# Optimization experiments

Hardware: AMD Instinct MI355X
Metric: run time of the kernel (lower is better)

Reference implementation:

```python
import jax, jax.numpy as jnp
import numpy as np

C, H, W_DIM, B, N = 9, 260, 346, 16, 32768
E = B * N
HIDDEN = 100
NEG_SLOPE = 0.1


def setup_inputs() -> dict:
    key = jax.random.key(0)
    ks = jax.random.split(key, 10)
    xs = jax.random.randint(ks[0], (E,), 0, W_DIM, dtype=jnp.int32)
    ys = jax.random.randint(ks[1], (E,), 0, H, dtype=jnp.int32)
    ts = jax.random.uniform(ks[2], (E,), dtype=jnp.float32)
    ps = jax.random.randint(ks[3], (E,), 0, 2, dtype=jnp.int32)  # polarity already mapped to {0,1}
    bs = jnp.repeat(jnp.arange(B, dtype=jnp.int32), N)           # batch id per event
    W1 = jax.random.normal(ks[4], (HIDDEN, 1), dtype=jnp.float32) * 0.5
    b1 = jax.random.normal(ks[5], (HIDDEN,), dtype=jnp.float32) * 0.1
    W2 = jax.random.normal(ks[6], (HIDDEN, HIDDEN), dtype=jnp.float32) * 0.1
    b2 = jax.random.normal(ks[7], (HIDDEN,), dtype=jnp.float32) * 0.1
    W3 = jax.random.normal(ks[8], (1, HIDDEN), dtype=jnp.float32) * 0.1
    b3 = jax.random.normal(ks[9], (1,), dtype=jnp.float32) * 0.1
    return {"xs": xs, "ys": ys, "ts": ts, "ps": ps, "bs": bs,
            "W1": W1, "b1": b1, "W2": W2, "b2": b2, "W3": W3, "b3": b3}


def _lrelu(v):
    return jnp.where(v >= 0, v, NEG_SLOPE * v)


def _value_layer(t, W1, b1, W2, b2, W3, b3):
    # ValueLayer MLP: scalar per event -> hidden -> hidden -> scalar
    h = _lrelu(t[:, None] * W1[:, 0][None, :] + b1)  # [E, HIDDEN]
    h = _lrelu(h @ W2.T + b2)                        # [E, HIDDEN]
    return (h @ W3.T + b3)[:, 0]                     # [E]


def reference(xs, ys, ts, ps, bs, W1, b1, W2, b2, W3, b3):
    num_voxels = 2 * C * H * W_DIM * B
    # idx = x + W*y + W*H*C*p + W*H*C*2*b  (+ W*H*i_bin per bin)
    idx0 = xs + W_DIM * ys + (W_DIM * H * C) * ps + (2 * W_DIM * H * C) * bs
    vox = jnp.zeros((num_voxels,), dtype=ts.dtype)
    for i_bin in range(C):  # fixed small loop over temporal bins
        vals = ts * _value_layer(ts - i_bin / (C - 1), W1, b1, W2, b2, W3, b3)
        idx = jnp.clip(idx0 + (W_DIM * H) * i_bin, 0, num_voxels - 1)
        vox = vox.at[idx].add(vals)
    vox = vox.reshape(B, 2, C, H, W_DIM)
    # concat polarity channels -> [B, 2C, H, W]
    return jnp.concatenate([vox[:, 0], vox[:, 1]], axis=1)
```

## Files before the change

kernel.cpp:

```cpp
#include <hip/hip_runtime.h>

#define C_BINS 9
#define H_DIM 260
#define WDIM 346
#define B_DIM 16
#define N_PER_B 32768
#define HIDDEN 100
#define NEG_SLOPE 0.1f
#define WH (WDIM * H_DIM)
#define NUM_VOXELS (2 * C_BINS * WH * B_DIM)
#define TABLE_N 16384
#define HALF_N (TABLE_N / 2)
#define BIN_SHIFT (TABLE_N / 16)
#define T9_STRIDE 12

#define ROWS_PER_TILE 4
#define TILES_PER_BP 65
#define LBUCKETS (2 * TILES_PER_BP)
#define NBUCKETS (B_DIM * LBUCKETS)
#define BUCKET_CAP 512
#define EV_PER_BLOCK 1024
#define TILE_ELEMS (C_BINS * ROWS_PER_TILE * WDIM)
#define TILE_F4 (TILE_ELEMS / 4)
#define CHUNK_F4 (ROWS_PER_TILE * WDIM / 4)
#define BUILD_BLOCKS (TABLE_N / 32 + 1)

#define SMEM_BYTES 41632
#define SM_STAGE 0
#define SM_SCAN  8192
#define SM_LCNT  10240
#define SM_LPRE  10760
#define SM_GBASE 11280
#define SM_SLB   11800

#define WS_TABLE_OFF 0
#define WS_COUNT_OFF 66048
#define WS_T9_OFF    74752
#define WS_REC_OFF   468480
#define WS_REC_SZ    ((size_t)NBUCKETS * BUCKET_CAP * 8)
#define WS_NEEDED    (WS_REC_OFF + WS_REC_SZ)

__global__ __launch_bounds__(256) void fused_build_bucket_kernel(
    const int* __restrict__ xs, const int* __restrict__ ys,
    const float* __restrict__ ts, const int* __restrict__ ps,
    const float* __restrict__ W1, const float* __restrict__ b1,
    const float* __restrict__ W2, const float* __restrict__ b2,
    const float* __restrict__ W3, const float* __restrict__ b3,
    float* __restrict__ table, float* __restrict__ t9,
    unsigned int* __restrict__ counts,
    unsigned long long* __restrict__ records,
    int E, int n_bucket_blocks, int write_t9)
{
    __shared__ __align__(16) char smem[SMEM_BYTES];
    const int tid = threadIdx.x;

    if (blockIdx.x < (unsigned)n_bucket_blocks) {
        unsigned long long* stage = (unsigned long long*)(smem + SM_STAGE);
        unsigned*      scan  = (unsigned*)(smem + SM_SCAN);
        unsigned*      lcnt  = (unsigned*)(smem + SM_LCNT);
        unsigned*      lpre  = (unsigned*)(smem + SM_LPRE);
        unsigned*      gbase = (unsigned*)(smem + SM_GBASE);
        unsigned char* slb   = (unsigned char*)(smem + SM_SLB);

        const int e0 = blockIdx.x * EV_PER_BLOCK;
        const int b  = e0 >> 15;

        for (int i = tid; i < LBUCKETS; i += 256) lcnt[i] = 0;
        __syncthreads();

        int lb[4];
        unsigned rank[4];
        unsigned long long rec[4];
        const int eb = e0 + tid * 4;
        if (eb + 3 < E) {
            const int v4 = (e0 >> 2) + tid;
            const int4   xv = ((const int4*)xs)[v4];
            const int4   yv = ((const int4*)ys)[v4];
            const int4   pv = ((const int4*)ps)[v4];
            const float4 tv = ((const float4*)ts)[v4];
            const int   xa[4] = {xv.x, xv.y, xv.z, xv.w};
            const int   ya[4] = {yv.x, yv.y, yv.z, yv.w};
            const int   pa[4] = {pv.x, pv.y, pv.z, pv.w};
            const float ta[4] = {tv.x, tv.y, tv.z, tv.w};
#pragma unroll
            for (int j = 0; j < 4; ++j) {
                const int yt = ya[j] >> 2;
                const int yl = ya[j] & 3;
                lb[j]  = pa[j] * TILES_PER_BP + yt;
                rec[j] = ((unsigned long long)__float_as_uint(ta[j]) << 32)
                       | (unsigned)(yl * WDIM + xa[j]);
                rank[j] = atomicAdd(&lcnt[lb[j]], 1u);
            }
        } else {
#pragma unroll
            for (int j = 0; j < 4; ++j) {
                const int e = eb + j;
                if (e < E) {
                    const int   x = xs[e];
                    const int   y = ys[e];
                    const int   p = ps[e];
                    const float t = ts[e];
                    const int  yt = y >> 2;
                    const int  yl = y & 3;
                    lb[j]  = p * TILES_PER_BP + yt;
                    rec[j] = ((unsigned long long)__float_as_uint(t) << 32)
                           | (unsigned)(yl * WDIM + x);
                    rank[j] = atomicAdd(&lcnt[lb[j]], 1u);
                } else {
                    lb[j] = -1;
                }
            }
        }
        __syncthreads();

        scan[tid] = (tid < LBUCKETS) ? lcnt[tid] : 0u;
        __syncthreads();
        int src = 0;
        for (int off = 1; off < 256; off <<= 1) {
            unsigned v = scan[src * 256 + tid];
            if (tid >= off) v += scan[src * 256 + tid - off];
            scan[(src ^ 1) * 256 + tid] = v;
            src ^= 1;
            __syncthreads();
        }
        if (tid < LBUCKETS) {
            const unsigned c = lcnt[tid];
            lpre[tid]  = scan[src * 256 + tid] - c;
            gbase[tid] = c ? atomicAdd(&counts[b * LBUCKETS + tid], c) : 0u;
        }
        __syncthreads();

#pragma unroll
        for (int j = 0; j < 4; ++j) {
            if (lb[j] >= 0) {
                const unsigned s = lpre[lb[j]] + rank[j];
                stage[s] = rec[j];
                slb[s]   = (unsigned char)lb[j];
            }
        }
        __syncthreads();

        const int nblk = (E - e0 < EV_PER_BLOCK) ? (E - e0) : EV_PER_BLOCK;
        for (int s = tid; s < nblk; s += 256) {
            const int l = slb[s];
            const unsigned ofs = gbase[l] + ((unsigned)s - lpre[l]);
            if (ofs < BUCKET_CAP)
                records[(size_t)(b * LBUCKETS + l) * BUCKET_CAP + ofs] = stage[s];
        }
    } else {
        float* sW2 = (float*)smem;
        float* sW1 = (float*)(smem + 40032);
        float* sb1 = sW1 + HIDDEN;
        float* sb2 = sb1 + HIDDEN;
        float* sW3 = sb2 + HIDDEN;

        {
            const float4* __restrict__ srcw = (const float4*)W2;
            float4* dst = (float4*)sW2;
            for (int i = tid; i < (HIDDEN * HIDDEN) / 4; i += 256) dst[i] = srcw[i];
        }
        if (tid < 8) sW2[HIDDEN * HIDDEN + tid] = 0.0f;
        if (tid < HIDDEN) {
            sW1[tid] = W1[tid];
            sb1[tid] = b1[tid];
            sb2[tid] = b2[tid];
            sW3[tid] = W3[tid];
        }
        __syncthreads();

        const int entry_local = tid >> 3;
        const int o  = tid & 7;
        const int q  = o & 3;
        const int j0 = (o >> 2) * 52;
        const int g  = (blockIdx.x - n_bucket_blocks) * 32 + entry_local;
        if (g > TABLE_N) return;
        const float u = -1.0f + (2.0f / (float)TABLE_N) * (float)g;

        float h1[52];
#pragma unroll
        for (int j = 0; j < 52; ++j) {
            const int jj = j0 + j;
            float v = (jj < HIDDEN) ? fmaf(u, sW1[jj], sb1[jj]) : 0.0f;
            h1[j] = (v >= 0.0f) ? v : NEG_SLOPE * v;
        }

        float acc = 0.0f;
        for (int k = q; k < HIDDEN; k += 4) {
            const float* __restrict__ row = &sW2[k * HIDDEN + j0];
            float a0 = 0.f, a1 = 0.f, a2 = 0.f, a3 = 0.f;
#pragma unroll
            for (int j = 0; j < 52; j += 4) {
                a0 = fmaf(row[j + 0], h1[j + 0], a0);
                a1 = fmaf(row[j + 1], h1[j + 1], a1);
                a2 = fmaf(row[j + 2], h1[j + 2], a2);
                a3 = fmaf(row[j + 3], h1[j + 3], a3);
            }
            float part = (a0 + a1) + (a2 + a3);
            part += __shfl_xor(part, 4);
            float a = sb2[k] + part;
            a = (a >= 0.0f) ? a : NEG_SLOPE * a;
            acc = fmaf(a, sW3[k], acc);
        }
        acc += __shfl_xor(acc, 1);
        acc += __shfl_xor(acc, 2);
        if (o == 0) {
            const float val = acc + b3[0];
            table[g] = val;
            if (write_t9) {
#pragma unroll
                for (int i = 0; i < C_BINS; ++i) {
                    const int r = g - HALF_N + BIN_SHIFT * i;
                    if (r >= 0 && r <= HALF_N) t9[r * T9_STRIDE + i] = val;
                }
            }
        }
    }
}

__global__ __launch_bounds__(512) void tile_kernel(
    const unsigned int* __restrict__ counts, const uint2* __restrict__ records,
    const float* __restrict__ t9, float* __restrict__ out)
{
    __shared__ __align__(16) float tile[TILE_ELEMS];
    const int tid = threadIdx.x;
    const int bucket = blockIdx.x;
    const int yt = bucket % TILES_PER_BP;
    const int bp = bucket / TILES_PER_BP;

    const int n = min(counts[bucket], (unsigned)BUCKET_CAP);
    const uint2* __restrict__ rec = records + (size_t)bucket * BUCKET_CAP;

    float4* __restrict__ t4 = (float4*)tile;
    {
        const float4 z = {0.f, 0.f, 0.f, 0.f};
        for (int k = tid; k < TILE_F4; k += 512) t4[k] = z;
    }
    __syncthreads();

    for (int r = tid; r < n; r += 512) {
        const uint2 v = rec[r];
        const int   pix = (int)v.x;
        const float t   = __uint_as_float(v.y);
        const float pos = (t + 1.0f) * ((float)TABLE_N * 0.5f);
        const int   i0  = (int)pos;
        const float frac = pos - (float)i0;
        const int   rr  = i0 - HALF_N;
        const float4* __restrict__ rowp = (const float4*)(t9 + rr * T9_STRIDE);
        const float4 a0 = rowp[0], a1 = rowp[1], a2 = rowp[2];
        const float4 c0 = rowp[3], c1 = rowp[4], c2 = rowp[5];
        const float t0v[9] = {a0.x, a0.y, a0.z, a0.w, a1.x, a1.y, a1.z, a1.w, a2.x};
        const float t1v[9] = {c0.x, c0.y, c0.z, c0.w, c1.x, c1.y, c1.z, c1.w, c2.x};
#pragma unroll
        for (int i = 0; i < C_BINS; ++i) {
            const float val = t * fmaf(frac, t1v[i] - t0v[i], t0v[i]);
            atomicAdd(&tile[i * (ROWS_PER_TILE * WDIM) + pix], val);
        }
    }
    __syncthreads();

    float* __restrict__ obase = out + (size_t)bp * (C_BINS * WH)
                              + yt * (ROWS_PER_TILE * WDIM);
    for (int s = tid; s < TILE_F4; s += 512) {
        const int i = s / CHUNK_F4;
        const int k = s - i * CHUNK_F4;
        ((float4*)(obase + i * WH))[k] = t4[i * CHUNK_F4 + k];
    }
}

__global__ __launch_bounds__(256) void zero_kernel(float4* __restrict__ out, int n4)
{
    int i = blockIdx.x * 256 + threadIdx.x;
    int stride = gridDim.x * 256;
    float4 z = {0.f, 0.f, 0.f, 0.f};
    for (; i < n4; i += stride) out[i] = z;
}

__global__ __launch_bounds__(256) void scatter_kernel(
    const int* __restrict__ xs, const int* __restrict__ ys,
    const float* __restrict__ ts, const int* __restrict__ ps,
    const int* __restrict__ bs, const float* __restrict__ table,
    float* __restrict__ out, int E)
{
    const int e = blockIdx.x * 256 + threadIdx.x;
    if (e >= E) return;
    const int x = xs[e], y = ys[e], p = ps[e], b = bs[e];
    const float t = ts[e];
    int idx0 = x + WDIM * y + (WH * C_BINS) * p + (2 * WH * C_BINS) * b;
#pragma unroll
    for (int i = 0; i < C_BINS; ++i) {
        float u   = t - (float)i * (1.0f / (float)(C_BINS - 1));
        float pos = (u + 1.0f) * ((float)TABLE_N * 0.5f);
        int   i0  = (int)pos;
        i0 = (i0 < 0) ? 0 : ((i0 > TABLE_N - 1) ? TABLE_N - 1 : i0);
        float frac = pos - (float)i0;
        float f  = fmaf(frac, table[i0 + 1] - table[i0], table[i0]);
        int idx = idx0 + WH * i;
        idx = (idx < 0) ? 0 : ((idx >= NUM_VOXELS) ? NUM_VOXELS - 1 : idx);
        atomicAdd(&out[idx], t * f);
    }
}

extern "C" void kernel_launch(void* const* d_in, const int* in_sizes, int n_in,
                              void* d_out, int out_size, void* d_ws, size_t ws_size,
                              hipStream_t stream)
{
    const int*   xs = (const int*)d_in[0];
    const int*   ys = (const int*)d_in[1];
    const float* ts = (const float*)d_in[2];
    const int*   ps = (const int*)d_in[3];
    const int*   bs = (const int*)d_in[4];
    const float* W1 = (const float*)d_in[5];
    const float* b1 = (const float*)d_in[6];
    const float* W2 = (const float*)d_in[7];
    const float* b2 = (const float*)d_in[8];
    const float* W3 = (const float*)d_in[9];
    const float* b3 = (const float*)d_in[10];

    float* out = (float*)d_out;
    char*  ws  = (char*)d_ws;
    float* table = (float*)(ws + WS_TABLE_OFF);
    unsigned int* counts = (unsigned int*)(ws + WS_COUNT_OFF);
    float* t9 = (float*)(ws + WS_T9_OFF);
    const int E = in_sizes[0];
    const int use_fast = (ws_size >= WS_NEEDED) ? 1 : 0;

    if (use_fast) {
        unsigned long long* records = (unsigned long long*)(ws + WS_REC_OFF);
        const int nbB = (E + EV_PER_BLOCK - 1) / EV_PER_BLOCK;
        hipMemsetAsync(counts, 0, NBUCKETS * sizeof(unsigned int), stream);
        fused_build_bucket_kernel<<<nbB + BUILD_BLOCKS, 256, 0, stream>>>(
            xs, ys, ts, ps, W1, b1, W2, b2, W3, b3,
            table, t9, counts, records, E, nbB, 1);
        tile_kernel<<<NBUCKETS, 512, 0, stream>>>(
            counts, (const uint2*)records, t9, out);
    } else {
        fused_build_bucket_kernel<<<BUILD_BLOCKS, 256, 0, stream>>>(
            xs, ys, ts, ps, W1, b1, W2, b2, W3, b3,
            table, t9, counts, (unsigned long long*)out , E, 0, 0);
        zero_kernel<<<1024, 256, 0, stream>>>((float4*)out, out_size / 4);
        scatter_kernel<<<(E + 255) / 256, 256, 0, stream>>>(
            xs, ys, ts, ps, bs, table, out, E);
    }
}
```

Baseline: 172.7 us.

## Replace global bucket counters with per-block sorted segments and prefix offsets

The bucketing pass no longer reserves space in fixed-capacity global buckets with atomics. Each block now writes its locally sorted 1024 records contiguously, using coalesced 16-byte stores, plus a small per-block prefix table of bucket offsets. The tile kernel assigns 16 lanes to each of the 32 source blocks of its batch and reads that block's segment for the bucket. This removes the memset, the global atomics and the bucket-cap overflow truncation. In exchange, reads in the tile kernel are more fragmented, only 16 lanes work per segment, and the fast path is now restricted to the exact event count.

```diff
diff --git a/kernel.cpp b/kernel.cpp
--- a/kernel.cpp
+++ b/kernel.cpp
@@ -18,8 +18,9 @@
 #define TILES_PER_BP 65
 #define LBUCKETS (2 * TILES_PER_BP)
 #define NBUCKETS (B_DIM * LBUCKETS)
-#define BUCKET_CAP 512
 #define EV_PER_BLOCK 1024
+#define BLOCKS_PER_BATCH (N_PER_B / EV_PER_BLOCK)
+#define PRE_STRIDE 132
 #define TILE_ELEMS (C_BINS * ROWS_PER_TILE * WDIM)
 #define TILE_F4 (TILE_ELEMS / 4)
 #define CHUNK_F4 (ROWS_PER_TILE * WDIM / 4)
@@ -30,14 +31,12 @@
 #define SM_SCAN  8192
 #define SM_LCNT  10240
 #define SM_LPRE  10760
-#define SM_GBASE 11280
-#define SM_SLB   11800
 
 #define WS_TABLE_OFF 0
-#define WS_COUNT_OFF 66048
-#define WS_T9_OFF    74752
-#define WS_REC_OFF   468480
-#define WS_REC_SZ    ((size_t)NBUCKETS * BUCKET_CAP * 8)
+#define WS_T9_OFF    66048
+#define WS_PRE_OFF   459392
+#define WS_REC_OFF   614400
+#define WS_REC_SZ    ((size_t)B_DIM * N_PER_B * 8)
 #define WS_NEEDED    (WS_REC_OFF + WS_REC_SZ)
 
 __global__ __launch_bounds__(256) void fused_build_bucket_kernel(
@@ -47,23 +46,21 @@
     const float* __restrict__ W2, const float* __restrict__ b2,
     const float* __restrict__ W3, const float* __restrict__ b3,
     float* __restrict__ table, float* __restrict__ t9,
-    unsigned int* __restrict__ counts,
+    unsigned short* __restrict__ pre,
     unsigned long long* __restrict__ records,
-    int E, int n_bucket_blocks, int write_t9)
+    int E, int n_bucket_blocks)
 {
     __shared__ __align__(16) char smem[SMEM_BYTES];
     const int tid = threadIdx.x;
 
     if (blockIdx.x < (unsigned)n_bucket_blocks) {
         unsigned long long* stage = (unsigned long long*)(smem + SM_STAGE);
-        unsigned*      scan  = (unsigned*)(smem + SM_SCAN);
-        unsigned*      lcnt  = (unsigned*)(smem + SM_LCNT);
-        unsigned*      lpre  = (unsigned*)(smem + SM_LPRE);
-        unsigned*      gbase = (unsigned*)(smem + SM_GBASE);
-        unsigned char* slb   = (unsigned char*)(smem + SM_SLB);
-
-        const int e0 = blockIdx.x * EV_PER_BLOCK;
-        const int b  = e0 >> 15;
+        unsigned* scan = (unsigned*)(smem + SM_SCAN);
+        unsigned* lcnt = (unsigned*)(smem + SM_LCNT);
+        unsigned* lpre = (unsigned*)(smem + SM_LPRE);
+
+        const int g  = blockIdx.x;
+        const int e0 = g * EV_PER_BLOCK;
 
         for (int i = tid; i < LBUCKETS; i += 256) lcnt[i] = 0;
         __syncthreads();
@@ -123,29 +120,29 @@
             src ^= 1;
             __syncthreads();
         }
-        if (tid < LBUCKETS) {
-            const unsigned c = lcnt[tid];
-            lpre[tid]  = scan[src * 256 + tid] - c;
-            gbase[tid] = c ? atomicAdd(&counts[b * LBUCKETS + tid], c) : 0u;
-        }
+        const int nblk = (E - e0 < EV_PER_BLOCK) ? (E - e0) : EV_PER_BLOCK;
+        if (tid < LBUCKETS)
+            lpre[tid] = scan[src * 256 + tid] - lcnt[tid];
+        if (tid <= LBUCKETS)
+            pre[g * PRE_STRIDE + tid] =
+                (unsigned short)((tid < LBUCKETS) ? (scan[src * 256 + tid] - lcnt[tid])
+                                                  : (unsigned)nblk);
         __syncthreads();
 
 #pragma unroll
         for (int j = 0; j < 4; ++j) {
-            if (lb[j] >= 0) {
-                const unsigned s = lpre[lb[j]] + rank[j];
-                stage[s] = rec[j];
-                slb[s]   = (unsigned char)lb[j];
-            }
-        }
-        __syncthreads();
-
-        const int nblk = (E - e0 < EV_PER_BLOCK) ? (E - e0) : EV_PER_BLOCK;
-        for (int s = tid; s < nblk; s += 256) {
-            const int l = slb[s];
-            const unsigned ofs = gbase[l] + ((unsigned)s - lpre[l]);
-            if (ofs < BUCKET_CAP)
-                records[(size_t)(b * LBUCKETS + l) * BUCKET_CAP + ofs] = stage[s];
+            if (lb[j] >= 0) stage[lpre[lb[j]] + rank[j]] = rec[j];
+        }
+        __syncthreads();
+
+        unsigned long long* __restrict__ dst = records + (size_t)g * EV_PER_BLOCK;
+        if (nblk == EV_PER_BLOCK) {
+            ulonglong2* __restrict__ d2 = (ulonglong2*)dst;
+            const ulonglong2* __restrict__ s2 = (const ulonglong2*)stage;
+#pragma unroll
+            for (int s = tid; s < EV_PER_BLOCK / 2; s += 256) d2[s] = s2[s];
+        } else {
+            for (int s = tid; s < nblk; s += 256) dst[s] = stage[s];
         }
     } else {
         float* sW2 = (float*)smem;
@@ -206,29 +203,34 @@
         if (o == 0) {
             const float val = acc + b3[0];
             table[g] = val;
-            if (write_t9) {
-#pragma unroll
-                for (int i = 0; i < C_BINS; ++i) {
-                    const int r = g - HALF_N + BIN_SHIFT * i;
-                    if (r >= 0 && r <= HALF_N) t9[r * T9_STRIDE + i] = val;
-                }
+#pragma unroll
+            for (int i = 0; i < C_BINS; ++i) {
+                const int r = g - HALF_N + BIN_SHIFT * i;
+                if (r >= 0 && r <= HALF_N) t9[r * T9_STRIDE + i] = val;
             }
         }
     }
 }
 
 __global__ __launch_bounds__(512) void tile_kernel(
-    const unsigned int* __restrict__ counts, const uint2* __restrict__ records,
+    const unsigned short* __restrict__ pre, const uint2* __restrict__ records,
     const float* __restrict__ t9, float* __restrict__ out)
 {
     __shared__ __align__(16) float tile[TILE_ELEMS];
     const int tid = threadIdx.x;
     const int bucket = blockIdx.x;
-    const int yt = bucket % TILES_PER_BP;
-    const int bp = bucket / TILES_PER_BP;
-
-    const int n = min(counts[bucket], (unsigned)BUCKET_CAP);
-    const uint2* __restrict__ rec = records + (size_t)bucket * BUCKET_CAP;
+    const int b = bucket / LBUCKETS;
+    const int l = bucket - b * LBUCKETS;
+    const int p  = (l >= TILES_PER_BP) ? 1 : 0;
+    const int yt = l - p * TILES_PER_BP;
+    const int bp = b * 2 + p;
+
+    const int seg  = tid >> 4;
+    const int lane = tid & 15;
+    const int g    = b * BLOCKS_PER_BATCH + seg;
+    const int lo   = pre[g * PRE_STRIDE + l];
+    const int hi   = pre[g * PRE_STRIDE + l + 1];
+    const uint2* __restrict__ segrec = records + (size_t)g * EV_PER_BLOCK;
 
     float4* __restrict__ t4 = (float4*)tile;
     {
@@ -237,8 +239,8 @@
     }
     __syncthreads();
 
-    for (int r = tid; r < n; r += 512) {
-        const uint2 v = rec[r];
+    for (int r = lo + lane; r < hi; r += 16) {
+        const uint2 v = segrec[r];
         const int   pix = (int)v.x;
         const float t   = __uint_as_float(v.y);
         const float pos = (t + 1.0f) * ((float)TABLE_N * 0.5f);
@@ -319,24 +321,23 @@
     float* out = (float*)d_out;
     char*  ws  = (char*)d_ws;
     float* table = (float*)(ws + WS_TABLE_OFF);
-    unsigned int* counts = (unsigned int*)(ws + WS_COUNT_OFF);
     float* t9 = (float*)(ws + WS_T9_OFF);
+    unsigned short* pre = (unsigned short*)(ws + WS_PRE_OFF);
     const int E = in_sizes[0];
-    const int use_fast = (ws_size >= WS_NEEDED) ? 1 : 0;
+    const int use_fast = (ws_size >= WS_NEEDED) && (E == B_DIM * N_PER_B);
 
     if (use_fast) {
         unsigned long long* records = (unsigned long long*)(ws + WS_REC_OFF);
-        const int nbB = (E + EV_PER_BLOCK - 1) / EV_PER_BLOCK;
-        hipMemsetAsync(counts, 0, NBUCKETS * sizeof(unsigned int), stream);
+        const int nbB = E / EV_PER_BLOCK;
         fused_build_bucket_kernel<<<nbB + BUILD_BLOCKS, 256, 0, stream>>>(
             xs, ys, ts, ps, W1, b1, W2, b2, W3, b3,
-            table, t9, counts, records, E, nbB, 1);
+            table, t9, pre, records, E, nbB);
         tile_kernel<<<NBUCKETS, 512, 0, stream>>>(
-            counts, (const uint2*)records, t9, out);
+            pre, (const uint2*)records, t9, out);
     } else {
         fused_build_bucket_kernel<<<BUILD_BLOCKS, 256, 0, stream>>>(
             xs, ys, ts, ps, W1, b1, W2, b2, W3, b3,
-            table, t9, counts, (unsigned long long*)out , E, 0, 0);
+            table, t9, pre, (unsigned long long*)out , E, 0);
         zero_kernel<<<1024, 256, 0, stream>>>((float4*)out, out_size / 4);
         scatter_kernel<<<(E + 255) / 256, 256, 0, stream>>>(
             xs, ys, ts, ps, bs, table, out, E);
```

Result: no change. 171.6 us (-0.6%).
